# Performance work log

Hardware: AMD Instinct MI355X
Metric: run time of the kernel (lower is better)

## Reference

```python
import jax, jax.numpy as jnp
import numpy as np

N_NODES = 50000
N_EDGES = 800000
HID = 64
F_NODE = 64
F_EDGE = 16
DEC_H = 64
EPS = 1e-5


def setup_inputs() -> dict:
    key = jax.random.key(0)
    ks = jax.random.split(key, 16)
    inp = {}
    inp['x'] = jax.random.normal(ks[0], (N_NODES, F_NODE), dtype=jnp.float32)
    inp['edge_index'] = jax.random.randint(ks[1], (2, N_EDGES), 0, N_NODES, dtype=jnp.int32)
    inp['edge_attr'] = jax.random.normal(ks[2], (N_EDGES, F_EDGE), dtype=jnp.float32)
    # 3 GCN layers (F_NODE == HID so weights stack)
    inp['conv_w'] = jax.random.normal(ks[3], (3, HID, HID), dtype=jnp.float32) / np.sqrt(HID)
    inp['conv_b'] = jnp.zeros((3, HID), dtype=jnp.float32)
    inp['ln_g'] = jnp.ones((3, HID), dtype=jnp.float32)
    inp['ln_b'] = jnp.zeros((3, HID), dtype=jnp.float32)
    dec_in = 2 * HID + F_EDGE
    inp['dec_w1'] = jax.random.normal(ks[4], (dec_in, DEC_H), dtype=jnp.float32) / np.sqrt(dec_in)
    inp['dec_b1'] = jnp.zeros((DEC_H,), dtype=jnp.float32)
    inp['dec_w2'] = jax.random.normal(ks[5], (DEC_H, DEC_H // 2), dtype=jnp.float32) / np.sqrt(DEC_H)
    inp['dec_b2'] = jnp.zeros((DEC_H // 2,), dtype=jnp.float32)
    inp['dec_w3'] = jax.random.normal(ks[6], (DEC_H // 2, 1), dtype=jnp.float32) / np.sqrt(DEC_H // 2)
    inp['dec_b3'] = jnp.zeros((1,), dtype=jnp.float32)
    return inp


def _layer_norm(h, g, b):
    mu = jnp.mean(h, axis=-1, keepdims=True)
    var = jnp.mean(jnp.square(h - mu), axis=-1, keepdims=True)
    return (h - mu) * jax.lax.rsqrt(var + EPS) * g + b


def _forward(x, edge_index, edge_attr, conv_w, conv_b, ln_g, ln_b,
             dec_w1, dec_b1, dec_w2, dec_b2, dec_w3, dec_b3):
    n = x.shape[0]
    src, dst = edge_index[0], edge_index[1]
    # add self-loops (PyG GCNConv default)
    loop = jnp.arange(n, dtype=edge_index.dtype)
    src_sl = jnp.concatenate([src, loop])
    dst_sl = jnp.concatenate([dst, loop])
    # symmetric normalization: deg over target column (incl. self-loops)
    deg = jax.ops.segment_sum(jnp.ones_like(src_sl, dtype=x.dtype), dst_sl, num_segments=n)
    dinv = jnp.where(deg > 0, jax.lax.rsqrt(deg), 0.0)
    norm = dinv[src_sl] * dinv[dst_sl]  # (E+N,)

    h = x
    for l in range(conv_w.shape[0]):
        t = h @ conv_w[l]                                   # (N, H)
        msg = t[src_sl] * norm[:, None]                     # (E+N, H)
        agg = jax.ops.segment_sum(msg, dst_sl, num_segments=n) + conv_b[l]
        h = jax.nn.relu(_layer_norm(agg, ln_g[l], ln_b[l]))
        # dropout is identity at inference

    # edge decoder: concat(src_emb, dst_emb, edge_attr) -> MLP -> scalar
    z = jnp.concatenate([h[src], h[dst], edge_attr], axis=-1)  # (E, 2H+Fe)
    z = jax.nn.relu(z @ dec_w1 + dec_b1)
    z = jax.nn.relu(z @ dec_w2 + dec_b2)
    return (z @ dec_w3 + dec_b3).squeeze(-1)                   # (E,)


def reference(x, edge_index, edge_attr, conv_w, conv_b, ln_g, ln_b,
              dec_w1, dec_b1, dec_w2, dec_b2, dec_w3, dec_b3):
    return _forward(x, edge_index, edge_attr, conv_w, conv_b, ln_g, ln_b,
                    dec_w1, dec_b1, dec_w2, dec_b2, dec_w3, dec_b3)
```

## Files before the change

kernel.cpp:

```cpp
#include <hip/hip_runtime.h>
#include <hip/hip_fp16.h>

#define N_NODES 50000
#define N_EDGES 800000
#define HID 64
#define F_EDGE 16
#define LN_EPS 1e-5f
#define SCAN_BLOCKS ((N_NODES + 255) / 256)

__device__ inline float wave_sum64(float v) {
    #pragma unroll
    for (int o = 32; o > 0; o >>= 1) v += __shfl_xor(v, o, 64);
    return v;
}

__global__ void k_zero_cnt(int* __restrict__ cnt) {
    int i = blockIdx.x * blockDim.x + threadIdx.x;
    if (i < N_NODES) cnt[i] = 0;
}

__global__ void k_count(const int* __restrict__ dst, int* __restrict__ cnt) {
    int e = blockIdx.x * blockDim.x + threadIdx.x;
    if (e < N_EDGES) atomicAdd(&cnt[dst[e]], 1);
}

__global__ void k_scan1(const int* __restrict__ cnt, int* __restrict__ row_ptr,
                        int* __restrict__ bsum, float* __restrict__ dinv) {
    __shared__ int wsum[4];
    int tid = threadIdx.x, lane = tid & 63, w = tid >> 6;
    int i = blockIdx.x * 256 + tid;
    int v = (i < N_NODES) ? cnt[i] : 0;
    if (i < N_NODES) dinv[i] = rsqrtf((float)v + 1.0f);
    int isc = v;
    #pragma unroll
    for (int o = 1; o < 64; o <<= 1) {
        int n = __shfl_up(isc, o, 64);
        if (lane >= o) isc += n;
    }
    if (lane == 63) wsum[w] = isc;
    __syncthreads();
    int woff = 0;
    #pragma unroll
    for (int k = 0; k < 4; k++) woff += (k < w) ? wsum[k] : 0;
    if (i < N_NODES) row_ptr[i] = woff + isc - v;
    if (tid == 255) bsum[blockIdx.x] = woff + isc;
}

__global__ void k_scan2(const int* __restrict__ bsum, int* __restrict__ boff) {
    __shared__ int wsum[4];
    int tid = threadIdx.x, lane = tid & 63, w = tid >> 6;
    int v = (tid < SCAN_BLOCKS) ? bsum[tid] : 0;
    int isc = v;
    #pragma unroll
    for (int o = 1; o < 64; o <<= 1) {
        int n = __shfl_up(isc, o, 64);
        if (lane >= o) isc += n;
    }
    if (lane == 63) wsum[w] = isc;
    __syncthreads();
    int woff = 0;
    #pragma unroll
    for (int k = 0; k < 4; k++) woff += (k < w) ? wsum[k] : 0;
    if (tid < SCAN_BLOCKS) boff[tid] = woff + isc - v;
}

__global__ void k_scan3(int* __restrict__ row_ptr, const int* __restrict__ boff,
                        int* __restrict__ cursor) {
    int i = blockIdx.x * blockDim.x + threadIdx.x;
    if (i < N_NODES) {
        int r = row_ptr[i] + boff[i >> 8];
        row_ptr[i] = r;
        cursor[i] = r;
    }
    if (i == 0) row_ptr[N_NODES] = N_EDGES;
}

__global__ void k_fill(const int* __restrict__ src, const int* __restrict__ dst,
                       int* __restrict__ cursor, int* __restrict__ col) {
    int e = blockIdx.x * blockDim.x + threadIdx.x;
    if (e < N_EDGES) {
        int s = src[e], d = dst[e];
        int pos = atomicAdd(&cursor[d], 1);
        col[pos] = s;
    }
}

__global__ void k_xs_init(const float* __restrict__ x, const float* __restrict__ dinv,
                          __half* __restrict__ xs) {
    int i = blockIdx.x * blockDim.x + threadIdx.x;
    if (i < N_NODES * 64) xs[i] = __float2half_rn(x[i] * dinv[i >> 6]);
}

__global__ void __launch_bounds__(256)
k_gather_agg(const __half* __restrict__ xs, const float* __restrict__ dinv,
             const int* __restrict__ row_ptr, const int* __restrict__ col,
             float* __restrict__ agg) {
    int gid = blockIdx.x * blockDim.x + threadIdx.x;
    int node = gid >> 6, lane = gid & 63;
    if (node >= N_NODES) return;
    int n0 = __builtin_amdgcn_readfirstlane(node);
    int q = lane >> 3;
    int c8 = lane & 7;
    const float4* x4 = (const float4*)xs;

    float acc[8];
    #pragma unroll
    for (int u = 0; u < 8; u++) acc[u] = 0.0f;

    if (q == 0) {
        float4 raw = x4[(size_t)n0 * 8 + c8];
        const __half2* hp = (const __half2*)&raw;
        float2 f0 = __half22float2(hp[0]);
        float2 f1 = __half22float2(hp[1]);
        float2 f2 = __half22float2(hp[2]);
        float2 f3 = __half22float2(hp[3]);
        acc[0] = f0.x; acc[1] = f0.y; acc[2] = f1.x; acc[3] = f1.y;
        acc[4] = f2.x; acc[5] = f2.y; acc[6] = f3.x; acc[7] = f3.y;
    }

    int beg = row_ptr[n0], end = row_ptr[n0 + 1];
    int deg = end - beg;

    int cL = 0;
    if (lane < deg) cL = col[beg + lane];
    int steps = (min(deg, 64) + 7) >> 3;

    #pragma unroll 4
    for (int st = 0; st < steps; st++) {
        int idx = 8 * st + q;
        int s = __shfl(cL, idx, 64);
        float m = (idx < deg) ? 1.0f : 0.0f;
        float4 raw = x4[(size_t)s * 8 + c8];
        const __half2* hp = (const __half2*)&raw;
        float2 f0 = __half22float2(hp[0]);
        float2 f1 = __half22float2(hp[1]);
        float2 f2 = __half22float2(hp[2]);
        float2 f3 = __half22float2(hp[3]);
        acc[0] = fmaf(f0.x, m, acc[0]); acc[1] = fmaf(f0.y, m, acc[1]);
        acc[2] = fmaf(f1.x, m, acc[2]); acc[3] = fmaf(f1.y, m, acc[3]);
        acc[4] = fmaf(f2.x, m, acc[4]); acc[5] = fmaf(f2.y, m, acc[5]);
        acc[6] = fmaf(f3.x, m, acc[6]); acc[7] = fmaf(f3.y, m, acc[7]);
    }
    for (int j = beg + 64 + q; j < end; j += 8) {
        int s = col[j];
        float4 raw = x4[(size_t)s * 8 + c8];
        const __half2* hp = (const __half2*)&raw;
        float2 f0 = __half22float2(hp[0]);
        float2 f1 = __half22float2(hp[1]);
        float2 f2 = __half22float2(hp[2]);
        float2 f3 = __half22float2(hp[3]);
        acc[0] += f0.x; acc[1] += f0.y; acc[2] += f1.x; acc[3] += f1.y;
        acc[4] += f2.x; acc[5] += f2.y; acc[6] += f3.x; acc[7] += f3.y;
    }

    #pragma unroll
    for (int o = 8; o <= 32; o <<= 1) {
        #pragma unroll
        for (int u = 0; u < 8; u++) acc[u] += __shfl_xor(acc[u], o, 64);
    }

    if (q == 0) {
        float di = dinv[n0];
        float4 y0, y1;
        y0.x = acc[0] * di; y0.y = acc[1] * di; y0.z = acc[2] * di; y0.w = acc[3] * di;
        y1.x = acc[4] * di; y1.y = acc[5] * di; y1.z = acc[6] * di; y1.w = acc[7] * di;
        float4* a4 = (float4*)agg;
        a4[(size_t)n0 * 16 + 2 * c8] = y0;
        a4[(size_t)n0 * 16 + 2 * c8 + 1] = y1;
    }
}

__global__ void __launch_bounds__(256)
k_gemm_ln(const float* __restrict__ agg, const float* __restrict__ W,
          const float* __restrict__ cb, const float* __restrict__ g,
          const float* __restrict__ b, const float* __restrict__ dinv,
          __half* __restrict__ xs_out, float* __restrict__ h_out) {
    int lane = threadIdx.x & 63;
    int wid = (blockIdx.x * blockDim.x + threadIdx.x) >> 6;
    int nwaves = (gridDim.x * blockDim.x) >> 6;
    float w[64];
    #pragma unroll
    for (int k = 0; k < 64; k++) w[k] = W[k * 64 + lane];
    float cbl = cb[lane], gl = g[lane], bl = b[lane];
    for (int row = wid; row < N_NODES; row += nwaves) {
        int r = __builtin_amdgcn_readfirstlane(row);
        const float* xr = agg + r * 64;
        float acc = cbl;
        #pragma unroll
        for (int k = 0; k < 64; k++) acc = fmaf(xr[k], w[k], acc);
        float mu = wave_sum64(acc) * (1.0f / 64.0f);
        float d = acc - mu;
        float var = wave_sum64(d * d) * (1.0f / 64.0f);
        float y = fmaxf(fmaf(d * rsqrtf(var + LN_EPS), gl, bl), 0.0f);
        if (xs_out) {
            xs_out[r * 64 + lane] = __float2half_rn(y * dinv[r]);
        } else {
            h_out[r * 64 + lane] = y;
        }
    }
}

__global__ void __launch_bounds__(256)
k_gemm_pq(const float* __restrict__ hin, const float* __restrict__ Wp,
          const float* __restrict__ bp, const float* __restrict__ Wq,
          __half* __restrict__ P, __half* __restrict__ Q) {
    int half_g = gridDim.x >> 1;
    bool isQ = (blockIdx.x >= half_g);
    const float* W = isQ ? Wq : Wp;
    __half* out = isQ ? Q : P;
    int lane = threadIdx.x & 63;
    int bid = isQ ? (blockIdx.x - half_g) : blockIdx.x;
    int wid = (bid * blockDim.x + threadIdx.x) >> 6;
    int nwaves = (half_g * blockDim.x) >> 6;
    float w[64];
    #pragma unroll
    for (int k = 0; k < 64; k++) w[k] = W[k * 64 + lane];
    float binit = isQ ? 0.0f : bp[lane];
    for (int row = wid; row < N_NODES; row += nwaves) {
        int r = __builtin_amdgcn_readfirstlane(row);
        const float* xr = hin + r * 64;
        float acc = binit;
        #pragma unroll
        for (int k = 0; k < 64; k++) acc = fmaf(xr[k], w[k], acc);
        out[r * 64 + lane] = __float2half_rn(acc);
    }
}

__global__ void __launch_bounds__(256)
k_decoder(const __half* __restrict__ P, const __half* __restrict__ Q,
          const int* __restrict__ src, const int* __restrict__ dst,
          const float* __restrict__ attr,
          const float* __restrict__ W1c,
          const float* __restrict__ W2, const float* __restrict__ b2,
          const float* __restrict__ W3, const float* __restrict__ b3,
          float* __restrict__ out) {
    int e = blockIdx.x * blockDim.x + threadIdx.x;
    if (e >= N_EDGES) return;
    int s = src[e], d = dst[e];

    const float4* ap = (const float4*)(attr + (size_t)e * 16);
    float4 av0 = ap[0], av1 = ap[1], av2 = ap[2], av3 = ap[3];

    float acc[64];
    const float4* Pp = (const float4*)(P + (size_t)s * 64);
    const float4* Qp = (const float4*)(Q + (size_t)d * 64);
    #pragma unroll
    for (int c = 0; c < 8; c++) {
        float4 pv = Pp[c], qv = Qp[c];
        const __half2* ph = (const __half2*)&pv;
        const __half2* qh = (const __half2*)&qv;
        #pragma unroll
        for (int u = 0; u < 4; u++) {
            float2 pf = __half22float2(ph[u]);
            float2 qf = __half22float2(qh[u]);
            acc[8 * c + 2 * u]     = pf.x + qf.x;
            acc[8 * c + 2 * u + 1] = pf.y + qf.y;
        }
    }

    #pragma unroll
    for (int j = 0; j < 64; j++) {
        float a = acc[j];
        a = fmaf(av0.x, W1c[0 * 64 + j], a);
        a = fmaf(av0.y, W1c[1 * 64 + j], a);
        a = fmaf(av0.z, W1c[2 * 64 + j], a);
        a = fmaf(av0.w, W1c[3 * 64 + j], a);
        a = fmaf(av1.x, W1c[4 * 64 + j], a);
        a = fmaf(av1.y, W1c[5 * 64 + j], a);
        a = fmaf(av1.z, W1c[6 * 64 + j], a);
        a = fmaf(av1.w, W1c[7 * 64 + j], a);
        a = fmaf(av2.x, W1c[8 * 64 + j], a);
        a = fmaf(av2.y, W1c[9 * 64 + j], a);
        a = fmaf(av2.z, W1c[10 * 64 + j], a);
        a = fmaf(av2.w, W1c[11 * 64 + j], a);
        a = fmaf(av3.x, W1c[12 * 64 + j], a);
        a = fmaf(av3.y, W1c[13 * 64 + j], a);
        a = fmaf(av3.z, W1c[14 * 64 + j], a);
        a = fmaf(av3.w, W1c[15 * 64 + j], a);
        acc[j] = fmaxf(a, 0.0f);
    }

    float acc2[32];
    #pragma unroll
    for (int j = 0; j < 32; j++) acc2[j] = b2[j];
    #pragma unroll
    for (int k = 0; k < 64; k++) {
        float hk = acc[k];
        #pragma unroll
        for (int j = 0; j < 32; j++)
            acc2[j] = fmaf(hk, W2[k * 32 + j], acc2[j]);
    }

    float o = b3[0];
    #pragma unroll
    for (int j = 0; j < 32; j++)
        o = fmaf(fmaxf(acc2[j], 0.0f), W3[j], o);
    out[e] = o;
}

extern "C" void kernel_launch(void* const* d_in, const int* in_sizes, int n_in,
                              void* d_out, int out_size, void* d_ws, size_t ws_size,
                              hipStream_t stream) {
    const float* x      = (const float*)d_in[0];
    const int*   ei     = (const int*)d_in[1];
    const float* attr   = (const float*)d_in[2];
    const float* conv_w = (const float*)d_in[3];
    const float* conv_b = (const float*)d_in[4];
    const float* ln_g   = (const float*)d_in[5];
    const float* ln_b   = (const float*)d_in[6];
    const float* dw1    = (const float*)d_in[7];
    const float* db1    = (const float*)d_in[8];
    const float* dw2    = (const float*)d_in[9];
    const float* db2    = (const float*)d_in[10];
    const float* dw3    = (const float*)d_in[11];
    const float* db3    = (const float*)d_in[12];
    float* out = (float*)d_out;

    const int* src = ei;
    const int* dst = ei + N_EDGES;

    char* p = (char*)d_ws;
    float*  dinv    = (float*)p;  p += sizeof(float) * N_NODES;
    float*  agg     = (float*)p;  p += sizeof(float) * (size_t)N_NODES * 64;
    float*  h3      = (float*)p;  p += sizeof(float) * (size_t)N_NODES * 64;
    __half* xs      = (__half*)p; p += sizeof(__half) * (size_t)N_NODES * 64;
    __half* P_h     = (__half*)p; p += sizeof(__half) * (size_t)N_NODES * 64;
    __half* Q_h     = (__half*)p; p += sizeof(__half) * (size_t)N_NODES * 64;
    int*    cnt     = (int*)p;    p += sizeof(int) * N_NODES;
    int*    cursor  = (int*)p;    p += sizeof(int) * N_NODES;
    int*    row_ptr = (int*)p;    p += sizeof(int) * (N_NODES + 1);
    int*    col     = (int*)p;    p += sizeof(int) * N_EDGES;
    int*    bsum    = (int*)p;    p += sizeof(int) * 256;
    int*    boff    = (int*)p;    p += sizeof(int) * 256;

    const int nb_nodes = (N_NODES + 255) / 256;
    const int nb_edges = (N_EDGES + 255) / 256;
    const int nb_elems = (N_NODES * 64 + 255) / 256;

    k_zero_cnt<<<nb_nodes, 256, 0, stream>>>(cnt);
    k_count<<<nb_edges, 256, 0, stream>>>(dst, cnt);
    k_scan1<<<SCAN_BLOCKS, 256, 0, stream>>>(cnt, row_ptr, bsum, dinv);
    k_scan2<<<1, 256, 0, stream>>>(bsum, boff);
    k_scan3<<<nb_nodes, 256, 0, stream>>>(row_ptr, boff, cursor);
    k_fill<<<nb_edges, 256, 0, stream>>>(src, dst, cursor, col);
    k_xs_init<<<nb_elems, 256, 0, stream>>>(x, dinv, xs);

    const int gemm_blocks = 1024;
    const int gather_blocks = N_NODES / 4;

    for (int l = 0; l < 3; l++) {
        k_gather_agg<<<gather_blocks, 256, 0, stream>>>(xs, dinv, row_ptr, col, agg);
        bool last = (l == 2);
        k_gemm_ln<<<gemm_blocks, 256, 0, stream>>>(
            agg, conv_w + l * 4096, conv_b + l * 64,
            ln_g + l * 64, ln_b + l * 64, dinv,
            last ? (__half*)nullptr : xs, last ? h3 : (float*)nullptr);
    }

    k_gemm_pq<<<2 * gemm_blocks, 256, 0, stream>>>(h3, dw1, db1, dw1 + 64 * 64, P_h, Q_h);

    k_decoder<<<nb_edges, 256, 0, stream>>>(
        P_h, Q_h, src, dst, attr, dw1 + 128 * 64, dw2, db2, dw3, db3, out);
}
```

Before: 465.7 us.

## Split node features into two column halves to shrink gather working set

```diff
diff --git a/kernel.cpp b/kernel.cpp
--- a/kernel.cpp
+++ b/kernel.cpp
@@ -7,6 +7,8 @@
 #define F_EDGE 16
 #define LN_EPS 1e-5f
 #define SCAN_BLOCKS ((N_NODES + 255) / 256)
+
+typedef float f4_native __attribute__((ext_vector_type(4)));
 
 __device__ inline float wave_sum64(float v) {
     #pragma unroll
@@ -86,29 +88,39 @@
 }
 
 __global__ void k_xs_init(const float* __restrict__ x, const float* __restrict__ dinv,
-                          __half* __restrict__ xs) {
+                          __half* __restrict__ xsA, __half* __restrict__ xsB) {
     int i = blockIdx.x * blockDim.x + threadIdx.x;
-    if (i < N_NODES * 64) xs[i] = __float2half_rn(x[i] * dinv[i >> 6]);
+    if (i < N_NODES * 64) {
+        int node = i >> 6, c = i & 63;
+        __half v = __float2half_rn(x[i] * dinv[node]);
+        if (c < 32) xsA[node * 32 + c] = v;
+        else        xsB[node * 32 + (c - 32)] = v;
+    }
 }
 
 __global__ void __launch_bounds__(256)
-k_gather_agg(const __half* __restrict__ xs, const float* __restrict__ dinv,
+k_gather_agg(const __half* __restrict__ xsA, const __half* __restrict__ xsB,
+             const float* __restrict__ dinv,
              const int* __restrict__ row_ptr, const int* __restrict__ col,
              float* __restrict__ agg) {
-    int gid = blockIdx.x * blockDim.x + threadIdx.x;
-    int node = gid >> 6, lane = gid & 63;
+    int b = blockIdx.x;
+    int half = (b >> 2) & 1;
+    int nodeBlock = (b >> 3) * 4 + (b & 3);
+    int wave = threadIdx.x >> 6, lane = threadIdx.x & 63;
+    int node = nodeBlock * 4 + wave;
     if (node >= N_NODES) return;
     int n0 = __builtin_amdgcn_readfirstlane(node);
-    int q = lane >> 3;
-    int c8 = lane & 7;
-    const float4* x4 = (const float4*)xs;
+    int slot = lane >> 2;
+    int cq = lane & 3;
+    const __half* xsH = half ? xsB : xsA;
+    const float4* x4 = (const float4*)xsH;
 
     float acc[8];
     #pragma unroll
     for (int u = 0; u < 8; u++) acc[u] = 0.0f;
 
-    if (q == 0) {
-        float4 raw = x4[(size_t)n0 * 8 + c8];
+    if (slot == 0) {
+        float4 raw = x4[(size_t)n0 * 4 + cq];
         const __half2* hp = (const __half2*)&raw;
         float2 f0 = __half22float2(hp[0]);
         float2 f1 = __half22float2(hp[1]);
@@ -122,15 +134,15 @@
     int deg = end - beg;
 
     int cL = 0;
-    if (lane < deg) cL = col[beg + lane];
-    int steps = (min(deg, 64) + 7) >> 3;
-
-    #pragma unroll 4
+    if (lane < deg) cL = __builtin_nontemporal_load(&col[beg + lane]);
+    int steps = (min(deg, 64) + 15) >> 4;
+
+    #pragma unroll 2
     for (int st = 0; st < steps; st++) {
-        int idx = 8 * st + q;
+        int idx = 16 * st + slot;
         int s = __shfl(cL, idx, 64);
         float m = (idx < deg) ? 1.0f : 0.0f;
-        float4 raw = x4[(size_t)s * 8 + c8];
+        float4 raw = x4[(size_t)s * 4 + cq];
         const __half2* hp = (const __half2*)&raw;
         float2 f0 = __half22float2(hp[0]);
         float2 f1 = __half22float2(hp[1]);
@@ -141,9 +153,9 @@
         acc[4] = fmaf(f2.x, m, acc[4]); acc[5] = fmaf(f2.y, m, acc[5]);
         acc[6] = fmaf(f3.x, m, acc[6]); acc[7] = fmaf(f3.y, m, acc[7]);
     }
-    for (int j = beg + 64 + q; j < end; j += 8) {
+    for (int j = beg + 64 + slot; j < end; j += 16) {
         int s = col[j];
-        float4 raw = x4[(size_t)s * 8 + c8];
+        float4 raw = x4[(size_t)s * 4 + cq];
         const __half2* hp = (const __half2*)&raw;
         float2 f0 = __half22float2(hp[0]);
         float2 f1 = __half22float2(hp[1]);
@@ -154,19 +166,20 @@
     }
 
     #pragma unroll
-    for (int o = 8; o <= 32; o <<= 1) {
+    for (int o = 4; o <= 32; o <<= 1) {
         #pragma unroll
         for (int u = 0; u < 8; u++) acc[u] += __shfl_xor(acc[u], o, 64);
     }
 
-    if (q == 0) {
+    if (slot == 0) {
         float di = dinv[n0];
-        float4 y0, y1;
+        f4_native y0, y1;
         y0.x = acc[0] * di; y0.y = acc[1] * di; y0.z = acc[2] * di; y0.w = acc[3] * di;
         y1.x = acc[4] * di; y1.y = acc[5] * di; y1.z = acc[6] * di; y1.w = acc[7] * di;
-        float4* a4 = (float4*)agg;
-        a4[(size_t)n0 * 16 + 2 * c8] = y0;
-        a4[(size_t)n0 * 16 + 2 * c8 + 1] = y1;
+        f4_native* a4 = (f4_native*)agg;
+        size_t base = (size_t)n0 * 16 + half * 8 + cq * 2;
+        __builtin_nontemporal_store(y0, &a4[base]);
+        __builtin_nontemporal_store(y1, &a4[base + 1]);
     }
 }
 
@@ -174,7 +187,8 @@
 k_gemm_ln(const float* __restrict__ agg, const float* __restrict__ W,
           const float* __restrict__ cb, const float* __restrict__ g,
           const float* __restrict__ b, const float* __restrict__ dinv,
-          __half* __restrict__ xs_out, float* __restrict__ h_out) {
+          __half* __restrict__ xsA, __half* __restrict__ xsB,
+          float* __restrict__ h_out) {
     int lane = threadIdx.x & 63;
     int wid = (blockIdx.x * blockDim.x + threadIdx.x) >> 6;
     int nwaves = (gridDim.x * blockDim.x) >> 6;
@@ -192,8 +206,10 @@
         float d = acc - mu;
         float var = wave_sum64(d * d) * (1.0f / 64.0f);
         float y = fmaxf(fmaf(d * rsqrtf(var + LN_EPS), gl, bl), 0.0f);
-        if (xs_out) {
-            xs_out[r * 64 + lane] = __float2half_rn(y * dinv[r]);
+        if (xsA) {
+            __half v = __float2half_rn(y * dinv[r]);
+            if (lane < 32) xsA[r * 32 + lane] = v;
+            else           xsB[r * 32 + (lane & 31)] = v;
         } else {
             h_out[r * 64 + lane] = y;
         }
@@ -323,7 +339,8 @@
     float*  dinv    = (float*)p;  p += sizeof(float) * N_NODES;
     float*  agg     = (float*)p;  p += sizeof(float) * (size_t)N_NODES * 64;
     float*  h3      = (float*)p;  p += sizeof(float) * (size_t)N_NODES * 64;
-    __half* xs      = (__half*)p; p += sizeof(__half) * (size_t)N_NODES * 64;
+    __half* xsA     = (__half*)p; p += sizeof(__half) * (size_t)N_NODES * 32;
+    __half* xsB     = (__half*)p; p += sizeof(__half) * (size_t)N_NODES * 32;
     __half* P_h     = (__half*)p; p += sizeof(__half) * (size_t)N_NODES * 64;
     __half* Q_h     = (__half*)p; p += sizeof(__half) * (size_t)N_NODES * 64;
     int*    cnt     = (int*)p;    p += sizeof(int) * N_NODES;
@@ -343,18 +360,19 @@
     k_scan2<<<1, 256, 0, stream>>>(bsum, boff);
     k_scan3<<<nb_nodes, 256, 0, stream>>>(row_ptr, boff, cursor);
     k_fill<<<nb_edges, 256, 0, stream>>>(src, dst, cursor, col);
-    k_xs_init<<<nb_elems, 256, 0, stream>>>(x, dinv, xs);
+    k_xs_init<<<nb_elems, 256, 0, stream>>>(x, dinv, xsA, xsB);
 
     const int gemm_blocks = 1024;
-    const int gather_blocks = N_NODES / 4;
+    const int gather_blocks = 2 * (N_NODES / 4);
 
     for (int l = 0; l < 3; l++) {
-        k_gather_agg<<<gather_blocks, 256, 0, stream>>>(xs, dinv, row_ptr, col, agg);
+        k_gather_agg<<<gather_blocks, 256, 0, stream>>>(xsA, xsB, dinv, row_ptr, col, agg);
         bool last = (l == 2);
         k_gemm_ln<<<gemm_blocks, 256, 0, stream>>>(
             agg, conv_w + l * 4096, conv_b + l * 64,
             ln_g + l * 64, ln_b + l * 64, dinv,
-            last ? (__half*)nullptr : xs, last ? h3 : (float*)nullptr);
+            last ? (__half*)nullptr : xsA, last ? (__half*)nullptr : xsB,
+            last ? h3 : (float*)nullptr);
     }
 
     k_gemm_pq<<<2 * gemm_blocks, 256, 0, stream>>>(h3, dw1, db1, dw1 + 64 * 64, P_h, Q_h);
```

Measured after the change: 538.7 us. 1.16x slower.
